# Performance work log

Measured on AMD Instinct MI355X. Metric: run time of the kernel, lower is better.

The kernel has to match this reference:

```python
import jax, jax.numpy as jnp
import numpy as np

B, T, E = 2, 2048, 1024
H, D = 8, 512
ROPE_BASE = 10000.0


def apply_rope(x):
    # x: [B, H, T, D] -- rotary positional embedding, half-split convention
    t = x.shape[2]
    d = x.shape[3]
    inv_freq = 1.0 / (ROPE_BASE ** (jnp.arange(0, d, 2, dtype=jnp.float32) / d))  # [D/2]
    ang = jnp.arange(t, dtype=jnp.float32)[:, None] * inv_freq[None, :]           # [T, D/2]
    cos = jnp.cos(ang)[None, None].astype(x.dtype)
    sin = jnp.sin(ang)[None, None].astype(x.dtype)
    x1, x2 = jnp.split(x, 2, axis=-1)
    return jnp.concatenate([x1 * cos - x2 * sin, x1 * sin + x2 * cos], axis=-1)


def setup_inputs() -> dict:
    key = jax.random.key(0)
    ks = jax.random.split(key, 5)
    s_in = 1.0 / np.sqrt(E)
    s_out = 1.0 / np.sqrt(H * D)
    return {
        "x": jax.random.normal(ks[0], (B, T, E), dtype=jnp.float32),
        "Wq": jax.random.normal(ks[1], (H * D, E), dtype=jnp.float32) * s_in,
        "Wk": jax.random.normal(ks[2], (H * D, E), dtype=jnp.float32) * s_in,
        "Wv": jax.random.normal(ks[3], (H * D, E), dtype=jnp.float32) * s_in,
        "Wo": jax.random.normal(ks[4], (E, H * D), dtype=jnp.float32) * s_out,
    }


def reference(x, Wq, Wk, Wv, Wo):
    b, t, e = x.shape
    # QKV projections (bias-free Linear: x @ W.T), reshape to [B, H, T, D]
    q = (x @ Wq.T).reshape(b, t, H, D).transpose(0, 2, 1, 3)
    k = (x @ Wk.T).reshape(b, t, H, D).transpose(0, 2, 1, 3)
    v = (x @ Wv.T).reshape(b, t, H, D).transpose(0, 2, 1, 3)
    # RoPE on q and k
    q = apply_rope(q)
    k = apply_rope(k)
    # scaled dot-product attention with causal mask
    scale = 1.0 / jnp.sqrt(jnp.asarray(D, dtype=x.dtype))
    scores = jnp.einsum("bhqd,bhkd->bhqk", q, k) * scale
    causal = jnp.tril(jnp.ones((t, t), dtype=bool))
    scores = jnp.where(causal[None, None], scores, jnp.asarray(-jnp.inf, dtype=scores.dtype))
    probs = jax.nn.softmax(scores, axis=-1)  # explicitly materialized, as in source
    attn = jnp.einsum("bhqk,bhkd->bhqd", probs, v)
    out = attn.transpose(0, 2, 1, 3).reshape(b, t, H * D) @ Wo.T
    return out
```

## Files before the change

kernel.cpp:

```cpp
#include <hip/hip_runtime.h>


#define DEV __device__ __forceinline__

using bf16x8  = __attribute__((ext_vector_type(8))) short;
using floatx4 = __attribute__((ext_vector_type(4))) float;

#define MFMA16(a, b, c) __builtin_amdgcn_mfma_f32_16x16x32_bf16((a), (b), (c), 0, 0, 0)

DEV unsigned short f2bf(float f) {
  union { float f; unsigned int u; } c; c.f = f;
  unsigned int u = c.u + 0x7FFFu + ((c.u >> 16) & 1u);
  return (unsigned short)(u >> 16);
}
DEV float bf2f(unsigned short h) {
  union { unsigned int u; float f; } c; c.u = ((unsigned int)h) << 16;
  return c.f;
}

DEV void ldsld16(const unsigned short* g, unsigned short* l) {
  __builtin_amdgcn_global_load_lds(
      (__attribute__((address_space(1))) void*)(g),
      (__attribute__((address_space(3))) void*)(l), 16, 0, 0);
}

__global__ void cast5_k(const float* __restrict__ x,  const float* __restrict__ wq,
                        const float* __restrict__ wk, const float* __restrict__ wv,
                        const float* __restrict__ wo,
                        unsigned short* __restrict__ xb,  unsigned short* __restrict__ wqb,
                        unsigned short* __restrict__ wkb, unsigned short* __restrict__ wvb,
                        unsigned short* __restrict__ wob) {
  const float* s; unsigned short* d;
  switch (blockIdx.y) {
    case 0: s = x;  d = xb;  break;
    case 1: s = wq; d = wqb; break;
    case 2: s = wk; d = wkb; break;
    case 3: s = wv; d = wvb; break;
    default: s = wo; d = wob; break;
  }
  int i = blockIdx.x * 256 + threadIdx.x;
  float4 v = ((const float4*)s)[i];
  uint2 o;
  o.x = (unsigned int)f2bf(v.x) | ((unsigned int)f2bf(v.y) << 16);
  o.y = (unsigned int)f2bf(v.z) | ((unsigned int)f2bf(v.w) << 16);
  ((uint2*)d)[i] = o;
}

__global__ __launch_bounds__(256) void qkv_gemm(
    const unsigned short* __restrict__ X,
    const unsigned short* __restrict__ Wq, const unsigned short* __restrict__ Wk,
    const unsigned short* __restrict__ Wv,
    unsigned short* __restrict__ Qo, unsigned short* __restrict__ Ko, unsigned short* __restrict__ Vo) {
  __shared__ __align__(16) unsigned short As[128 * 32];
  __shared__ __align__(16) unsigned short Bs[128 * 32];
  const int tid = threadIdx.x;
  const int wave = tid >> 6, lane = tid & 63, quad = lane >> 4, l16 = lane & 15;
  const int m0 = blockIdx.x * 128, n0 = blockIdx.y * 128;
  const int z = blockIdx.z;
  const unsigned short* W = (z == 0) ? Wq : (z == 1) ? Wk : Wv;
  const int wm = (wave >> 1) * 64, wn = (wave & 1) * 64;
  floatx4 acc[4][4];
#pragma unroll
  for (int i = 0; i < 4; ++i)
#pragma unroll
    for (int j = 0; j < 4; ++j) acc[i][j] = (floatx4){0.f, 0.f, 0.f, 0.f};

  const int r0 = wave * 32;
  const int lrow = lane >> 2, lchunk = (lane & 3) * 8;
  for (int k0 = 0; k0 < 1024; k0 += 32) {
    const unsigned short* ga = X + (size_t)(m0 + r0 + lrow) * 1024 + k0 + lchunk;
    const unsigned short* gb = W + (size_t)(n0 + r0 + lrow) * 1024 + k0 + lchunk;
    ldsld16(ga, As + r0 * 32);
    ldsld16(ga + (size_t)16 * 1024, As + r0 * 32 + 512);
    ldsld16(gb, Bs + r0 * 32);
    ldsld16(gb + (size_t)16 * 1024, Bs + r0 * 32 + 512);
    __syncthreads();
    bf16x8 af[4], bw[4];
#pragma unroll
    for (int i = 0; i < 4; ++i) af[i] = *(const bf16x8*)(As + (wm + i * 16 + l16) * 32 + quad * 8);
#pragma unroll
    for (int j = 0; j < 4; ++j) bw[j] = *(const bf16x8*)(Bs + (wn + j * 16 + l16) * 32 + quad * 8);
#pragma unroll
    for (int i = 0; i < 4; ++i)
#pragma unroll
      for (int j = 0; j < 4; ++j) acc[i][j] = MFMA16(af[i], bw[j], acc[i][j]);
    __syncthreads();
  }
#pragma unroll
  for (int i = 0; i < 4; ++i)
#pragma unroll
    for (int j = 0; j < 4; ++j) {
      int gn = n0 + wn + j * 16 + l16;
      int h = gn >> 9, d = gn & 511;
#pragma unroll
      for (int r = 0; r < 4; ++r) {
        int gm = m0 + wm + i * 16 + quad * 4 + r;
        int b = gm >> 11, t = gm & 2047;
        unsigned short v = f2bf(acc[i][j][r]);
        if (z == 2)
          Vo[((size_t)((b * 8 + h) * 512 + d)) * 2048 + t] = v;
        else
          ((z == 0) ? Qo : Ko)[((size_t)((b * 8 + h) * 2048 + t)) * 512 + d] = v;
      }
    }
}

__global__ void rope_k(unsigned short* __restrict__ Q, unsigned short* __restrict__ K) {
  int idx = blockIdx.x * 256 + threadIdx.x;
  unsigned short* P = (idx & 8388608) ? K : Q;
  int r = idx & 8388607;
  int row = r >> 8;
  int i = r & 255;
  int t = row & 2047;
  size_t base = (size_t)row * 512;
  float x1 = bf2f(P[base + i]);
  float x2 = bf2f(P[base + i + 256]);
  float freq = expf(-(float)i * 0.03597789207803197f);
  float ang = (float)t * freq;
  float sv, cv;
  sincosf(ang, &sv, &cv);
  P[base + i]       = f2bf(x1 * cv - x2 * sv);
  P[base + i + 256] = f2bf(x1 * sv + x2 * cv);
}

__global__ __launch_bounds__(256) void flash_attn(
    const unsigned short* __restrict__ Q, const unsigned short* __restrict__ K,
    const unsigned short* __restrict__ Vt, unsigned short* __restrict__ attn,
    unsigned short* __restrict__ P1, float* __restrict__ ml1, float* __restrict__ ml2,
    int split) {
  __shared__ __align__(16) unsigned short Ks[32 * 264];
  __shared__ __align__(16) unsigned short Vs[512 * 40];
  __shared__ __align__(16) unsigned short Ps[4 * 16 * 32];
  const int tid = threadIdx.x;
  const int wave = tid >> 6, lane = tid & 63, quad = lane >> 4, l16 = lane & 15;
  const int bh = blockIdx.x, b = bh >> 3, h = bh & 7;
  const int y = blockIdx.y;
  int qi, st0, stN, om;
  if (split) {
    if (y < 16)      { qi = 31 - y;  st0 = 0;  stN = 32;         om = 1; }
    else if (y < 32) { qi = 47 - y;  st0 = 32; stN = 2 * qi + 2; om = 2; }
    else             { qi = 47 - y;  st0 = 0;  stN = 2 * qi + 2; om = 0; }
  } else {
    qi = (y < 16) ? (31 - y) : (y - 16);
    st0 = 0; stN = 2 * qi + 2; om = 0;
  }
  const size_t bhoff = ((size_t)bh) << 20;
  const unsigned short* Qp = Q + bhoff;
  const unsigned short* Kp = K + bhoff;
  const unsigned short* Vp = Vt + bhoff;
  const int qb = qi * 64;

  bf16x8 qf[16];
  {
    const unsigned short* qrow = Qp + (size_t)(qb + wave * 16 + l16) * 512 + quad * 8;
#pragma unroll
    for (int ks = 0; ks < 16; ++ks) qf[ks] = *(const bf16x8*)(qrow + ks * 32);
  }
  floatx4 o[32];
#pragma unroll
  for (int n = 0; n < 32; ++n) o[n] = (floatx4){0.f, 0.f, 0.f, 0.f};
  float m_[4], l_[4];
#pragma unroll
  for (int r = 0; r < 4; ++r) { m_[r] = -3.0e38f; l_[r] = 0.f; }

  for (int st = st0; st < stN; ++st) {
    const int s0 = st * 32;
#pragma unroll
    for (int it = 0; it < 8; ++it) {
      int cid = it * 256 + tid;
      int d = cid >> 2, c = cid & 3;
      *(bf16x8*)(Vs + d * 40 + c * 8) = *(const bf16x8*)(Vp + (size_t)d * 2048 + s0 + c * 8);
    }
#pragma unroll
    for (int it = 0; it < 4; ++it) {
      int cid = it * 256 + tid;
      int row = cid >> 5, cc = cid & 31;
      *(bf16x8*)(Ks + row * 264 + cc * 8) = *(const bf16x8*)(Kp + (size_t)(s0 + row) * 512 + cc * 8);
    }
    __syncthreads();
    floatx4 sc0 = (floatx4){0.f, 0.f, 0.f, 0.f}, sc1 = sc0;
#pragma unroll
    for (int ks = 0; ks < 8; ++ks) {
      bf16x8 k0v = *(const bf16x8*)(Ks + l16 * 264 + ks * 32 + quad * 8);
      bf16x8 k1v = *(const bf16x8*)(Ks + (16 + l16) * 264 + ks * 32 + quad * 8);
      sc0 = MFMA16(qf[ks], k0v, sc0);
      sc1 = MFMA16(qf[ks], k1v, sc1);
    }
    __syncthreads();
#pragma unroll
    for (int it = 0; it < 4; ++it) {
      int cid = it * 256 + tid;
      int row = cid >> 5, cc = cid & 31;
      *(bf16x8*)(Ks + row * 264 + cc * 8) = *(const bf16x8*)(Kp + (size_t)(s0 + row) * 512 + 256 + cc * 8);
    }
    __syncthreads();
#pragma unroll
    for (int ks = 0; ks < 8; ++ks) {
      bf16x8 k0v = *(const bf16x8*)(Ks + l16 * 264 + ks * 32 + quad * 8);
      bf16x8 k1v = *(const bf16x8*)(Ks + (16 + l16) * 264 + ks * 32 + quad * 8);
      sc0 = MFMA16(qf[8 + ks], k0v, sc0);
      sc1 = MFMA16(qf[8 + ks], k1v, sc1);
    }
    const float scale = 0.04419417382415922f;
    const int qrow0 = qb + wave * 16 + quad * 4;
    float pr0[4], pr1[4], mr[4];
#pragma unroll
    for (int r = 0; r < 4; ++r) {
      float a0 = sc0[r] * scale, a1 = sc1[r] * scale;
      if (s0 + l16 > qrow0 + r) a0 = -3.0e38f;
      if (s0 + 16 + l16 > qrow0 + r) a1 = -3.0e38f;
      pr0[r] = a0; pr1[r] = a1;
      mr[r] = fmaxf(a0, a1);
    }
#pragma unroll
    for (int off = 1; off < 16; off <<= 1)
#pragma unroll
      for (int r = 0; r < 4; ++r) mr[r] = fmaxf(mr[r], __shfl_xor(mr[r], off, 64));
    float alpha[4], rs[4];
#pragma unroll
    for (int r = 0; r < 4; ++r) {
      float mn = fmaxf(m_[r], mr[r]);
      alpha[r] = __expf(m_[r] - mn);
      m_[r] = mn;
      float p0 = __expf(pr0[r] - mn);
      float p1 = __expf(pr1[r] - mn);
      rs[r] = p0 + p1;
      Ps[wave * 512 + (quad * 4 + r) * 32 + l16] = f2bf(p0);
      Ps[wave * 512 + (quad * 4 + r) * 32 + 16 + l16] = f2bf(p1);
    }
#pragma unroll
    for (int off = 1; off < 16; off <<= 1)
#pragma unroll
      for (int r = 0; r < 4; ++r) rs[r] += __shfl_xor(rs[r], off, 64);
#pragma unroll
    for (int r = 0; r < 4; ++r) l_[r] = l_[r] * alpha[r] + rs[r];
    if (__any(alpha[0] + alpha[1] + alpha[2] + alpha[3] < 4.0f)) {
#pragma unroll
      for (int n = 0; n < 32; ++n)
#pragma unroll
        for (int r = 0; r < 4; ++r) o[n][r] *= alpha[r];
    }
    bf16x8 pf = *(const bf16x8*)(Ps + wave * 512 + l16 * 32 + quad * 8);
#pragma unroll
    for (int nt = 0; nt < 32; ++nt) {
      bf16x8 vf = *(const bf16x8*)(Vs + (nt * 16 + l16) * 40 + quad * 8);
      o[nt] = MFMA16(pf, vf, o[nt]);
    }
    __syncthreads();
  }
  const int rowi = wave * 16 + quad * 4;
  if (om == 0) {
    float inv[4];
#pragma unroll
    for (int r = 0; r < 4; ++r) inv[r] = 1.0f / l_[r];
    unsigned short* arow = attn + ((size_t)(b * 2048 + qb + rowi)) * 4096 + h * 512 + l16;
#pragma unroll
    for (int nt = 0; nt < 32; ++nt)
#pragma unroll
      for (int r = 0; r < 4; ++r)
        arow[(size_t)r * 4096 + nt * 16] = f2bf(o[nt][r] * inv[r]);
  } else {
    const int p = bh * 16 + (qi - 16);
    float* ml = (om == 1) ? ml1 : ml2;
    if (l16 == 0) {
#pragma unroll
      for (int r = 0; r < 4; ++r) {
        ml[(size_t)p * 128 + (rowi + r) * 2]     = m_[r];
        ml[(size_t)p * 128 + (rowi + r) * 2 + 1] = l_[r];
      }
    }
    if (om == 1) {
      unsigned short* prow = P1 + ((size_t)p * 64 + rowi) * 512 + l16;
#pragma unroll
      for (int nt = 0; nt < 32; ++nt)
#pragma unroll
        for (int r = 0; r < 4; ++r)
          prow[(size_t)r * 512 + nt * 16] = f2bf(o[nt][r]);
    } else {
      unsigned short* arow = attn + ((size_t)(b * 2048 + qb + rowi)) * 4096 + h * 512 + l16;
#pragma unroll
      for (int nt = 0; nt < 32; ++nt)
#pragma unroll
        for (int r = 0; r < 4; ++r)
          arow[(size_t)r * 4096 + nt * 16] = f2bf(o[nt][r]);
    }
  }
}

__global__ void combine_k(const unsigned short* __restrict__ P1,
                          const float* __restrict__ ml1, const float* __restrict__ ml2,
                          unsigned short* __restrict__ attn) {
  const int p = blockIdx.x;
  const int bh = p >> 4, b = bh >> 3, h = bh & 7, qi = 16 + (p & 15);
  const int tid = threadIdx.x;
#pragma unroll
  for (int it = 0; it < 16; ++it) {
    int idx = it * 256 + tid;
    int r = idx >> 6, dc = idx & 63;
    float m1 = ml1[(size_t)p * 128 + r * 2], l1 = ml1[(size_t)p * 128 + r * 2 + 1];
    float m2 = ml2[(size_t)p * 128 + r * 2], l2 = ml2[(size_t)p * 128 + r * 2 + 1];
    float M = fmaxf(m1, m2);
    float w1 = __expf(m1 - M), w2 = __expf(m2 - M);
    float inv = 1.0f / (l1 * w1 + l2 * w2);
    const unsigned short* o1 = P1 + ((size_t)p * 64 + r) * 512 + dc * 8;
    unsigned short* ap = attn + ((size_t)(b * 2048 + qi * 64 + r)) * 4096 + h * 512 + dc * 8;
    unsigned short res[8];
#pragma unroll
    for (int j = 0; j < 8; ++j)
      res[j] = f2bf((bf2f(o1[j]) * w1 + bf2f(ap[j]) * w2) * inv);
    *(bf16x8*)ap = *(bf16x8*)res;
  }
}

__global__ __launch_bounds__(256) void out_gemm(
    const unsigned short* __restrict__ A, const unsigned short* __restrict__ W,
    float* __restrict__ C) {
  __shared__ __align__(16) unsigned short As[128 * 32];
  __shared__ __align__(16) unsigned short Bs[128 * 32];
  const int tid = threadIdx.x;
  const int wave = tid >> 6, lane = tid & 63, quad = lane >> 4, l16 = lane & 15;
  const int m0 = blockIdx.x * 128, n0 = blockIdx.y * 128;
  const int kb = blockIdx.z * 1024;
  const int wm = (wave >> 1) * 64, wn = (wave & 1) * 64;
  floatx4 acc[4][4];
#pragma unroll
  for (int i = 0; i < 4; ++i)
#pragma unroll
    for (int j = 0; j < 4; ++j) acc[i][j] = (floatx4){0.f, 0.f, 0.f, 0.f};
  const int r0 = wave * 32;
  const int lrow = lane >> 2, lchunk = (lane & 3) * 8;
  for (int k0 = kb; k0 < kb + 1024; k0 += 32) {
    const unsigned short* ga = A + (size_t)(m0 + r0 + lrow) * 4096 + k0 + lchunk;
    const unsigned short* gb = W + (size_t)(n0 + r0 + lrow) * 4096 + k0 + lchunk;
    ldsld16(ga, As + r0 * 32);
    ldsld16(ga + (size_t)16 * 4096, As + r0 * 32 + 512);
    ldsld16(gb, Bs + r0 * 32);
    ldsld16(gb + (size_t)16 * 4096, Bs + r0 * 32 + 512);
    __syncthreads();
    bf16x8 af[4], bw[4];
#pragma unroll
    for (int i = 0; i < 4; ++i) af[i] = *(const bf16x8*)(As + (wm + i * 16 + l16) * 32 + quad * 8);
#pragma unroll
    for (int j = 0; j < 4; ++j) bw[j] = *(const bf16x8*)(Bs + (wn + j * 16 + l16) * 32 + quad * 8);
#pragma unroll
    for (int i = 0; i < 4; ++i)
#pragma unroll
      for (int j = 0; j < 4; ++j) acc[i][j] = MFMA16(af[i], bw[j], acc[i][j]);
    __syncthreads();
  }
#pragma unroll
  for (int i = 0; i < 4; ++i)
#pragma unroll
    for (int j = 0; j < 4; ++j) {
      int gn = n0 + wn + j * 16 + l16;
#pragma unroll
      for (int r = 0; r < 4; ++r) {
        int gm = m0 + wm + i * 16 + quad * 4 + r;
        unsafeAtomicAdd(&C[(size_t)gm * 1024 + gn], acc[i][j][r]);
      }
    }
}

extern "C" void kernel_launch(void* const* d_in, const int* in_sizes, int n_in,
                              void* d_out, int out_size, void* d_ws, size_t ws_size,
                              hipStream_t stream) {
  const float* x  = (const float*)d_in[0];
  const float* Wq = (const float*)d_in[1];
  const float* Wk = (const float*)d_in[2];
  const float* Wv = (const float*)d_in[3];
  const float* Wo = (const float*)d_in[4];
  float* out = (float*)d_out;
  char* ws = (char*)d_ws;
  const size_t MB = 1048576;
  unsigned short* xb    = (unsigned short*)(ws + 0 * MB);
  unsigned short* wqb   = (unsigned short*)(ws + 8 * MB);
  unsigned short* wkb   = (unsigned short*)(ws + 16 * MB);
  unsigned short* wvb   = (unsigned short*)(ws + 24 * MB);
  unsigned short* wob   = (unsigned short*)(ws + 32 * MB);
  unsigned short* Qb    = (unsigned short*)(ws + 40 * MB);
  unsigned short* Kb    = (unsigned short*)(ws + 72 * MB);
  unsigned short* Vb    = (unsigned short*)(ws + 104 * MB);
  unsigned short* attnb = (unsigned short*)(ws + 0 * MB);
  unsigned short* P1    = (unsigned short*)(ws + 136 * MB);
  float* ml1            = (float*)(ws + 152 * MB);
  float* ml2            = (float*)(ws + 152 * MB + 131072);
  const int split = (ws_size >= (size_t)160 * MB) ? 1 : 0;

  hipMemsetAsync(d_out, 0, (size_t)4096 * 1024 * 4, stream);

  cast5_k<<<dim3(4096, 5), 256, 0, stream>>>(x, Wq, Wk, Wv, Wo, xb, wqb, wkb, wvb, wob);
  qkv_gemm<<<dim3(32, 32, 3), 256, 0, stream>>>(xb, wqb, wkb, wvb, Qb, Kb, Vb);
  rope_k<<<65536, 256, 0, stream>>>(Qb, Kb);
  flash_attn<<<dim3(16, split ? 48 : 32), 256, 0, stream>>>(Qb, Kb, Vb, attnb, P1, ml1, ml2, split);
  if (split) combine_k<<<256, 256, 0, stream>>>(P1, ml1, ml2, attnb);
  out_gemm<<<dim3(32, 8, 4), 256, 0, stream>>>(attnb, wob, out);
}
```

Before: 680.0 us.

## Restructure flash attention to 32-row tiles with split-D waves and slab V layout

The attention kernel now processes 32 query rows per block. Four waves split both the rows and the 512-wide head dimension, and each pair of waves sums its partial QK^T scores through shared memory. K fragments are read straight from global memory instead of being staged in LDS, and V is written by the QKV GEMM in 32-token slab blocks so each tile can be copied into LDS with asynchronous global_load_lds and prefetched for the next step. Split-K partitioning is rebalanced per q-tile, and occupancy is raised with launch_bounds(256,3). This trades extra block syncs, an LDS reduction and uncached direct K loads for lower register pressure, more blocks and less LDS staging.

```diff
diff --git a/kernel.cpp b/kernel.cpp
--- a/kernel.cpp
+++ b/kernel.cpp
@@ -92,15 +92,19 @@
     for (int j = 0; j < 4; ++j) {
       int gn = n0 + wn + j * 16 + l16;
       int h = gn >> 9, d = gn & 511;
-#pragma unroll
-      for (int r = 0; r < 4; ++r) {
-        int gm = m0 + wm + i * 16 + quad * 4 + r;
-        int b = gm >> 11, t = gm & 2047;
-        unsigned short v = f2bf(acc[i][j][r]);
-        if (z == 2)
-          Vo[((size_t)((b * 8 + h) * 512 + d)) * 2048 + t] = v;
-        else
-          ((z == 0) ? Qo : Ko)[((size_t)((b * 8 + h) * 2048 + t)) * 512 + d] = v;
+      int gm0 = m0 + wm + i * 16 + quad * 4;
+      int b = gm0 >> 11, t0 = gm0 & 2047;
+      if (z == 2) {
+        unsigned short pk[4];
+#pragma unroll
+        for (int r = 0; r < 4; ++r) pk[r] = f2bf(acc[i][j][r]);
+        size_t off = ((size_t)((b * 8 + h) * 64 + (t0 >> 5))) * 16384 + (size_t)d * 32 + (t0 & 31);
+        *(uint2*)(Vo + off) = *(uint2*)pk;
+      } else {
+        unsigned short* P = (z == 0) ? Qo : Ko;
+        size_t base = ((size_t)((b * 8 + h) * 2048 + t0)) * 512 + d;
+#pragma unroll
+        for (int r = 0; r < 4; ++r) P[base + (size_t)r * 512] = f2bf(acc[i][j][r]);
       }
     }
 }
@@ -123,93 +127,94 @@
   P[base + i + 256] = f2bf(x1 * sv + x2 * cv);
 }
 
-__global__ __launch_bounds__(256) void flash_attn(
+__global__ __launch_bounds__(256, 3) void flash_attn(
     const unsigned short* __restrict__ Q, const unsigned short* __restrict__ K,
-    const unsigned short* __restrict__ Vt, unsigned short* __restrict__ attn,
+    const unsigned short* __restrict__ Vslab, unsigned short* __restrict__ attn,
     unsigned short* __restrict__ P1, float* __restrict__ ml1, float* __restrict__ ml2,
     int split) {
-  __shared__ __align__(16) unsigned short Ks[32 * 264];
-  __shared__ __align__(16) unsigned short Vs[512 * 40];
-  __shared__ __align__(16) unsigned short Ps[4 * 16 * 32];
+  __shared__ __align__(16) unsigned short Vs[512 * 32];
+  __shared__ __align__(16) unsigned short Ps[2 * 512];
+  __shared__ __align__(16) float Sred[2 * 2 * 512];
   const int tid = threadIdx.x;
   const int wave = tid >> 6, lane = tid & 63, quad = lane >> 4, l16 = lane & 15;
-  const int bh = blockIdx.x, b = bh >> 3, h = bh & 7;
+  const int pr = wave >> 1, hh = wave & 1;
+  const int bh = blockIdx.x, b = bh >> 3, head = bh & 7;
   const int y = blockIdx.y;
   int qi, st0, stN, om;
   if (split) {
-    if (y < 16)      { qi = 31 - y;  st0 = 0;  stN = 32;         om = 1; }
-    else if (y < 32) { qi = 47 - y;  st0 = 32; stN = 2 * qi + 2; om = 2; }
-    else             { qi = 47 - y;  st0 = 0;  stN = 2 * qi + 2; om = 0; }
-  } else {
-    qi = (y < 16) ? (31 - y) : (y - 16);
-    st0 = 0; stN = 2 * qi + 2; om = 0;
-  }
-  const size_t bhoff = ((size_t)bh) << 20;
+    if (y < 64) {
+      qi = 63 - (y >> 1);
+      int mid = (qi + 1) >> 1;
+      if ((y & 1) == 0) { st0 = 0;   stN = mid;    om = 1; }
+      else              { st0 = mid; stN = qi + 1; om = 2; }
+    } else { qi = 95 - y; st0 = 0; stN = qi + 1; om = 0; }
+  } else { qi = 63 - y; st0 = 0; stN = qi + 1; om = 0; }
+
+  const size_t bhoff = (size_t)bh << 20;
   const unsigned short* Qp = Q + bhoff;
   const unsigned short* Kp = K + bhoff;
-  const unsigned short* Vp = Vt + bhoff;
-  const int qb = qi * 64;
-
-  bf16x8 qf[16];
+  const unsigned short* Vp = Vslab + bhoff;
+  const int qb = qi * 32;
+
+  bf16x8 qf[8];
   {
-    const unsigned short* qrow = Qp + (size_t)(qb + wave * 16 + l16) * 512 + quad * 8;
-#pragma unroll
-    for (int ks = 0; ks < 16; ++ks) qf[ks] = *(const bf16x8*)(qrow + ks * 32);
-  }
-  floatx4 o[32];
-#pragma unroll
-  for (int n = 0; n < 32; ++n) o[n] = (floatx4){0.f, 0.f, 0.f, 0.f};
+    const unsigned short* qrow = Qp + (size_t)(qb + pr * 16 + l16) * 512 + hh * 256 + quad * 8;
+#pragma unroll
+    for (int ks = 0; ks < 8; ++ks) qf[ks] = *(const bf16x8*)(qrow + ks * 32);
+  }
+  floatx4 o[16];
+#pragma unroll
+  for (int n = 0; n < 16; ++n) o[n] = (floatx4){0.f, 0.f, 0.f, 0.f};
   float m_[4], l_[4];
 #pragma unroll
   for (int r = 0; r < 4; ++r) { m_[r] = -3.0e38f; l_[r] = 0.f; }
+
+  {
+    const unsigned short* g = Vp + (size_t)st0 * 16384 + (size_t)(wave * 8) * 512 + lane * 8;
+    unsigned short* lp = Vs + wave * 8 * 512;
+#pragma unroll
+    for (int i = 0; i < 8; ++i) ldsld16(g + i * 512, lp + i * 512);
+  }
 
   for (int st = st0; st < stN; ++st) {
     const int s0 = st * 32;
-#pragma unroll
-    for (int it = 0; it < 8; ++it) {
-      int cid = it * 256 + tid;
-      int d = cid >> 2, c = cid & 3;
-      *(bf16x8*)(Vs + d * 40 + c * 8) = *(const bf16x8*)(Vp + (size_t)d * 2048 + s0 + c * 8);
-    }
-#pragma unroll
-    for (int it = 0; it < 4; ++it) {
-      int cid = it * 256 + tid;
-      int row = cid >> 5, cc = cid & 31;
-      *(bf16x8*)(Ks + row * 264 + cc * 8) = *(const bf16x8*)(Kp + (size_t)(s0 + row) * 512 + cc * 8);
-    }
-    __syncthreads();
     floatx4 sc0 = (floatx4){0.f, 0.f, 0.f, 0.f}, sc1 = sc0;
-#pragma unroll
-    for (int ks = 0; ks < 8; ++ks) {
-      bf16x8 k0v = *(const bf16x8*)(Ks + l16 * 264 + ks * 32 + quad * 8);
-      bf16x8 k1v = *(const bf16x8*)(Ks + (16 + l16) * 264 + ks * 32 + quad * 8);
-      sc0 = MFMA16(qf[ks], k0v, sc0);
-      sc1 = MFMA16(qf[ks], k1v, sc1);
-    }
-    __syncthreads();
-#pragma unroll
-    for (int it = 0; it < 4; ++it) {
-      int cid = it * 256 + tid;
-      int row = cid >> 5, cc = cid & 31;
-      *(bf16x8*)(Ks + row * 264 + cc * 8) = *(const bf16x8*)(Kp + (size_t)(s0 + row) * 512 + 256 + cc * 8);
-    }
-    __syncthreads();
-#pragma unroll
-    for (int ks = 0; ks < 8; ++ks) {
-      bf16x8 k0v = *(const bf16x8*)(Ks + l16 * 264 + ks * 32 + quad * 8);
-      bf16x8 k1v = *(const bf16x8*)(Ks + (16 + l16) * 264 + ks * 32 + quad * 8);
-      sc0 = MFMA16(qf[8 + ks], k0v, sc0);
-      sc1 = MFMA16(qf[8 + ks], k1v, sc1);
+    const unsigned short* kbase = Kp + hh * 256 + quad * 8;
+#pragma unroll
+    for (int half = 0; half < 2; ++half) {
+      bf16x8 kb[8];
+#pragma unroll
+      for (int q4 = 0; q4 < 4; ++q4) {
+        int ks = half * 4 + q4;
+        kb[q4 * 2]     = *(const bf16x8*)(kbase + (size_t)(s0 + l16) * 512 + ks * 32);
+        kb[q4 * 2 + 1] = *(const bf16x8*)(kbase + (size_t)(s0 + 16 + l16) * 512 + ks * 32);
+      }
+#pragma unroll
+      for (int q4 = 0; q4 < 4; ++q4) {
+        sc0 = MFMA16(qf[half * 4 + q4], kb[q4 * 2], sc0);
+        sc1 = MFMA16(qf[half * 4 + q4], kb[q4 * 2 + 1], sc1);
+      }
+    }
+    float* sw = Sred + (pr * 2 + hh) * 512;
+    *(floatx4*)(sw + l16 * 16 + quad * 4) = sc0;
+    *(floatx4*)(sw + (16 + l16) * 16 + quad * 4) = sc1;
+    __syncthreads();
+    {
+      const float* srd = Sred + (pr * 2 + (1 - hh)) * 512;
+      floatx4 r0 = *(const floatx4*)(srd + l16 * 16 + quad * 4);
+      floatx4 r1 = *(const floatx4*)(srd + (16 + l16) * 16 + quad * 4);
+#pragma unroll
+      for (int r = 0; r < 4; ++r) { sc0[r] += r0[r]; sc1[r] += r1[r]; }
     }
     const float scale = 0.04419417382415922f;
-    const int qrow0 = qb + wave * 16 + quad * 4;
-    float pr0[4], pr1[4], mr[4];
+    const int qrow0 = qb + pr * 16 + quad * 4;
+    float pv0[4], pv1[4], mr[4];
 #pragma unroll
     for (int r = 0; r < 4; ++r) {
       float a0 = sc0[r] * scale, a1 = sc1[r] * scale;
       if (s0 + l16 > qrow0 + r) a0 = -3.0e38f;
       if (s0 + 16 + l16 > qrow0 + r) a1 = -3.0e38f;
-      pr0[r] = a0; pr1[r] = a1;
+      pv0[r] = a0; pv1[r] = a1;
       mr[r] = fmaxf(a0, a1);
     }
 #pragma unroll
@@ -222,11 +227,10 @@
       float mn = fmaxf(m_[r], mr[r]);
       alpha[r] = __expf(m_[r] - mn);
       m_[r] = mn;
-      float p0 = __expf(pr0[r] - mn);
-      float p1 = __expf(pr1[r] - mn);
+      float p0 = __expf(pv0[r] - mn);
+      float p1 = __expf(pv1[r] - mn);
       rs[r] = p0 + p1;
-      Ps[wave * 512 + (quad * 4 + r) * 32 + l16] = f2bf(p0);
-      Ps[wave * 512 + (quad * 4 + r) * 32 + 16 + l16] = f2bf(p1);
+      Ps[pr * 512 + (quad * 4 + r) * 32 + hh * 16 + l16] = f2bf(hh ? p1 : p0);
     }
 #pragma unroll
     for (int off = 1; off < 16; off <<= 1)
@@ -234,55 +238,62 @@
       for (int r = 0; r < 4; ++r) rs[r] += __shfl_xor(rs[r], off, 64);
 #pragma unroll
     for (int r = 0; r < 4; ++r) l_[r] = l_[r] * alpha[r] + rs[r];
+    __syncthreads();
     if (__any(alpha[0] + alpha[1] + alpha[2] + alpha[3] < 4.0f)) {
 #pragma unroll
-      for (int n = 0; n < 32; ++n)
+      for (int n = 0; n < 16; ++n)
 #pragma unroll
         for (int r = 0; r < 4; ++r) o[n][r] *= alpha[r];
     }
-    bf16x8 pf = *(const bf16x8*)(Ps + wave * 512 + l16 * 32 + quad * 8);
-#pragma unroll
-    for (int nt = 0; nt < 32; ++nt) {
-      bf16x8 vf = *(const bf16x8*)(Vs + (nt * 16 + l16) * 40 + quad * 8);
+    bf16x8 pf = *(const bf16x8*)(Ps + pr * 512 + l16 * 32 + quad * 8);
+#pragma unroll
+    for (int nt = 0; nt < 16; ++nt) {
+      bf16x8 vf = *(const bf16x8*)(Vs + (size_t)(hh * 256 + nt * 16 + l16) * 32 + quad * 8);
       o[nt] = MFMA16(pf, vf, o[nt]);
     }
     __syncthreads();
-  }
-  const int rowi = wave * 16 + quad * 4;
-  if (om == 0) {
-    float inv[4];
-#pragma unroll
-    for (int r = 0; r < 4; ++r) inv[r] = 1.0f / l_[r];
-    unsigned short* arow = attn + ((size_t)(b * 2048 + qb + rowi)) * 4096 + h * 512 + l16;
-#pragma unroll
-    for (int nt = 0; nt < 32; ++nt)
+    if (st + 1 < stN) {
+      const unsigned short* g = Vp + (size_t)(st + 1) * 16384 + (size_t)(wave * 8) * 512 + lane * 8;
+      unsigned short* lp = Vs + wave * 8 * 512;
+#pragma unroll
+      for (int i = 0; i < 8; ++i) ldsld16(g + i * 512, lp + i * 512);
+    }
+  }
+  const int rbase = pr * 16 + quad * 4;
+  int p1i = bh * 32 + (qi - 32);
+  if (om == 1) {
+    unsigned short* prow = P1 + ((size_t)p1i * 32 + rbase) * 512 + hh * 256 + l16;
+#pragma unroll
+    for (int nt = 0; nt < 16; ++nt)
 #pragma unroll
       for (int r = 0; r < 4; ++r)
-        arow[(size_t)r * 4096 + nt * 16] = f2bf(o[nt][r] * inv[r]);
+        prow[(size_t)r * 512 + nt * 16] = f2bf(o[nt][r]);
   } else {
-    const int p = bh * 16 + (qi - 16);
-    float* ml = (om == 1) ? ml1 : ml2;
-    if (l16 == 0) {
-#pragma unroll
-      for (int r = 0; r < 4; ++r) {
-        ml[(size_t)p * 128 + (rowi + r) * 2]     = m_[r];
-        ml[(size_t)p * 128 + (rowi + r) * 2 + 1] = l_[r];
-      }
-    }
-    if (om == 1) {
-      unsigned short* prow = P1 + ((size_t)p * 64 + rowi) * 512 + l16;
-#pragma unroll
-      for (int nt = 0; nt < 32; ++nt)
+    unsigned short* arow =
+        attn + ((size_t)(b * 2048 + qb + rbase)) * 4096 + head * 512 + hh * 256 + l16;
+    if (om == 0) {
+      float inv[4];
+#pragma unroll
+      for (int r = 0; r < 4; ++r) inv[r] = 1.0f / l_[r];
+#pragma unroll
+      for (int nt = 0; nt < 16; ++nt)
 #pragma unroll
         for (int r = 0; r < 4; ++r)
-          prow[(size_t)r * 512 + nt * 16] = f2bf(o[nt][r]);
+          arow[(size_t)r * 4096 + nt * 16] = f2bf(o[nt][r] * inv[r]);
     } else {
-      unsigned short* arow = attn + ((size_t)(b * 2048 + qb + rowi)) * 4096 + h * 512 + l16;
-#pragma unroll
-      for (int nt = 0; nt < 32; ++nt)
+#pragma unroll
+      for (int nt = 0; nt < 16; ++nt)
 #pragma unroll
         for (int r = 0; r < 4; ++r)
           arow[(size_t)r * 4096 + nt * 16] = f2bf(o[nt][r]);
+    }
+  }
+  if (om != 0 && hh == 0 && l16 == 0) {
+    float* ml = (om == 1) ? ml1 : ml2;
+#pragma unroll
+    for (int r = 0; r < 4; ++r) {
+      ml[(size_t)p1i * 64 + (rbase + r) * 2]     = m_[r];
+      ml[(size_t)p1i * 64 + (rbase + r) * 2 + 1] = l_[r];
     }
   }
 }
@@ -291,19 +302,19 @@
                           const float* __restrict__ ml1, const float* __restrict__ ml2,
                           unsigned short* __restrict__ attn) {
   const int p = blockIdx.x;
-  const int bh = p >> 4, b = bh >> 3, h = bh & 7, qi = 16 + (p & 15);
+  const int bh = p >> 5, qi = 32 + (p & 31), b = bh >> 3, head = bh & 7;
   const int tid = threadIdx.x;
 #pragma unroll
-  for (int it = 0; it < 16; ++it) {
+  for (int it = 0; it < 8; ++it) {
     int idx = it * 256 + tid;
-    int r = idx >> 6, dc = idx & 63;
-    float m1 = ml1[(size_t)p * 128 + r * 2], l1 = ml1[(size_t)p * 128 + r * 2 + 1];
-    float m2 = ml2[(size_t)p * 128 + r * 2], l2 = ml2[(size_t)p * 128 + r * 2 + 1];
+    int row = idx >> 6, c8 = (idx & 63) * 8;
+    float m1 = ml1[(size_t)p * 64 + row * 2], l1 = ml1[(size_t)p * 64 + row * 2 + 1];
+    float m2 = ml2[(size_t)p * 64 + row * 2], l2 = ml2[(size_t)p * 64 + row * 2 + 1];
     float M = fmaxf(m1, m2);
     float w1 = __expf(m1 - M), w2 = __expf(m2 - M);
     float inv = 1.0f / (l1 * w1 + l2 * w2);
-    const unsigned short* o1 = P1 + ((size_t)p * 64 + r) * 512 + dc * 8;
-    unsigned short* ap = attn + ((size_t)(b * 2048 + qi * 64 + r)) * 4096 + h * 512 + dc * 8;
+    const unsigned short* o1 = P1 + ((size_t)p * 32 + row) * 512 + c8;
+    unsigned short* ap = attn + ((size_t)(b * 2048 + qi * 32 + row)) * 4096 + head * 512 + c8;
     unsigned short res[8];
 #pragma unroll
     for (int j = 0; j < 8; ++j)
@@ -391,7 +402,7 @@
   cast5_k<<<dim3(4096, 5), 256, 0, stream>>>(x, Wq, Wk, Wv, Wo, xb, wqb, wkb, wvb, wob);
   qkv_gemm<<<dim3(32, 32, 3), 256, 0, stream>>>(xb, wqb, wkb, wvb, Qb, Kb, Vb);
   rope_k<<<65536, 256, 0, stream>>>(Qb, Kb);
-  flash_attn<<<dim3(16, split ? 48 : 32), 256, 0, stream>>>(Qb, Kb, Vb, attnb, P1, ml1, ml2, split);
-  if (split) combine_k<<<256, 256, 0, stream>>>(P1, ml1, ml2, attnb);
+  flash_attn<<<dim3(16, split ? 96 : 64), 256, 0, stream>>>(Qb, Kb, Vb, attnb, P1, ml1, ml2, split);
+  if (split) combine_k<<<512, 256, 0, stream>>>(P1, ml1, ml2, attnb);
   out_gemm<<<dim3(32, 8, 4), 256, 0, stream>>>(attnb, wob, out);
 }
```

After: 704.4 us. +3.6%, slower.

## Pre-tile K/V into padded LDS layout and async-prefetch tiles in flash attention

Applied to the files above, without the earlier changes.

The QKV GEMM now writes K and V straight into a per-tile padded layout that matches the attention kernel's LDS layout. The attention kernel can then fill LDS with direct global-to-LDS loads of the whole 32x512 K tile at once, and it prefetches the next tile after each iteration's compute. This removes the split K halves, the extra barriers and the register-staged copies. It also pads the P buffer, sets launch_bounds for two blocks, and moves the Wo cast later so workspace can be reused. The cost is more LDS per block, and the next-tile loads overlap only with the loop tail, since the barrier sits at the loop top.

```diff
diff --git a/kernel.cpp b/kernel.cpp
--- a/kernel.cpp
+++ b/kernel.cpp
@@ -7,6 +7,12 @@
 using floatx4 = __attribute__((ext_vector_type(4))) float;
 
 #define MFMA16(a, b, c) __builtin_amdgcn_mfma_f32_16x16x32_bf16((a), (b), (c), 0, 0, 0)
+
+#define KT_BH 1097728
+#define KT_TILE 17152
+#define KT_ROW 536
+#define VT_BH 1310720
+#define VT_TILE 20480
 
 DEV unsigned short f2bf(float f) {
   union { float f; unsigned int u; } c; c.f = f;
@@ -24,20 +30,26 @@
       (__attribute__((address_space(3))) void*)(l), 16, 0, 0);
 }
 
-__global__ void cast5_k(const float* __restrict__ x,  const float* __restrict__ wq,
+__global__ void cast4_k(const float* __restrict__ x,  const float* __restrict__ wq,
                         const float* __restrict__ wk, const float* __restrict__ wv,
-                        const float* __restrict__ wo,
                         unsigned short* __restrict__ xb,  unsigned short* __restrict__ wqb,
-                        unsigned short* __restrict__ wkb, unsigned short* __restrict__ wvb,
-                        unsigned short* __restrict__ wob) {
+                        unsigned short* __restrict__ wkb, unsigned short* __restrict__ wvb) {
   const float* s; unsigned short* d;
   switch (blockIdx.y) {
     case 0: s = x;  d = xb;  break;
     case 1: s = wq; d = wqb; break;
     case 2: s = wk; d = wkb; break;
-    case 3: s = wv; d = wvb; break;
-    default: s = wo; d = wob; break;
-  }
+    default: s = wv; d = wvb; break;
+  }
+  int i = blockIdx.x * 256 + threadIdx.x;
+  float4 v = ((const float4*)s)[i];
+  uint2 o;
+  o.x = (unsigned int)f2bf(v.x) | ((unsigned int)f2bf(v.y) << 16);
+  o.y = (unsigned int)f2bf(v.z) | ((unsigned int)f2bf(v.w) << 16);
+  ((uint2*)d)[i] = o;
+}
+
+__global__ void cast1_k(const float* __restrict__ s, unsigned short* __restrict__ d) {
   int i = blockIdx.x * 256 + threadIdx.x;
   float4 v = ((const float4*)s)[i];
   uint2 o;
@@ -92,27 +104,43 @@
     for (int j = 0; j < 4; ++j) {
       int gn = n0 + wn + j * 16 + l16;
       int h = gn >> 9, d = gn & 511;
-#pragma unroll
-      for (int r = 0; r < 4; ++r) {
-        int gm = m0 + wm + i * 16 + quad * 4 + r;
-        int b = gm >> 11, t = gm & 2047;
-        unsigned short v = f2bf(acc[i][j][r]);
-        if (z == 2)
-          Vo[((size_t)((b * 8 + h) * 512 + d)) * 2048 + t] = v;
-        else
-          ((z == 0) ? Qo : Ko)[((size_t)((b * 8 + h) * 2048 + t)) * 512 + d] = v;
+      int gm0 = m0 + wm + i * 16 + quad * 4;
+      int b = gm0 >> 11, t0 = gm0 & 2047;
+      int bh = b * 8 + h;
+      if (z == 2) {
+        unsigned short pk[4];
+#pragma unroll
+        for (int r = 0; r < 4; ++r) pk[r] = f2bf(acc[i][j][r]);
+        size_t off = (size_t)bh * VT_BH + (t0 >> 5) * VT_TILE + (size_t)d * 40 + (t0 & 31);
+        *(uint2*)(Vo + off) = *(uint2*)pk;
+      } else if (z == 1) {
+        size_t off = (size_t)bh * KT_BH + (t0 >> 5) * KT_TILE + (size_t)(t0 & 31) * KT_ROW + d;
+#pragma unroll
+        for (int r = 0; r < 4; ++r) Ko[off + (size_t)r * KT_ROW] = f2bf(acc[i][j][r]);
+      } else {
+        size_t base = ((size_t)(bh * 2048 + t0)) * 512 + d;
+#pragma unroll
+        for (int r = 0; r < 4; ++r) Qo[base + (size_t)r * 512] = f2bf(acc[i][j][r]);
       }
     }
 }
 
-__global__ void rope_k(unsigned short* __restrict__ Q, unsigned short* __restrict__ K) {
+__global__ void rope_k(unsigned short* __restrict__ Q, unsigned short* __restrict__ Kt) {
   int idx = blockIdx.x * 256 + threadIdx.x;
-  unsigned short* P = (idx & 8388608) ? K : Q;
   int r = idx & 8388607;
   int row = r >> 8;
   int i = r & 255;
   int t = row & 2047;
-  size_t base = (size_t)row * 512;
+  unsigned short* P;
+  size_t base;
+  if (idx & 8388608) {
+    int bh = row >> 11;
+    base = (size_t)bh * KT_BH + (t >> 5) * KT_TILE + (size_t)(t & 31) * KT_ROW;
+    P = Kt;
+  } else {
+    base = (size_t)row * 512;
+    P = Q;
+  }
   float x1 = bf2f(P[base + i]);
   float x2 = bf2f(P[base + i + 256]);
   float freq = expf(-(float)i * 0.03597789207803197f);
@@ -123,31 +151,28 @@
   P[base + i + 256] = f2bf(x1 * sv + x2 * cv);
 }
 
-__global__ __launch_bounds__(256) void flash_attn(
-    const unsigned short* __restrict__ Q, const unsigned short* __restrict__ K,
+__global__ __launch_bounds__(256, 2) void flash_attn(
+    const unsigned short* __restrict__ Q, const unsigned short* __restrict__ Kt,
     const unsigned short* __restrict__ Vt, unsigned short* __restrict__ attn,
     unsigned short* __restrict__ P1, float* __restrict__ ml1, float* __restrict__ ml2,
     int split) {
-  __shared__ __align__(16) unsigned short Ks[32 * 264];
+  __shared__ __align__(16) unsigned short Ks[32 * 536];
   __shared__ __align__(16) unsigned short Vs[512 * 40];
-  __shared__ __align__(16) unsigned short Ps[4 * 16 * 32];
+  __shared__ __align__(16) unsigned short Ps[4 * 16 * 40];
   const int tid = threadIdx.x;
   const int wave = tid >> 6, lane = tid & 63, quad = lane >> 4, l16 = lane & 15;
-  const int bh = blockIdx.x, b = bh >> 3, h = bh & 7;
+  const int bh = blockIdx.x, b = bh >> 3, head = bh & 7;
   const int y = blockIdx.y;
   int qi, st0, stN, om;
   if (split) {
-    if (y < 16)      { qi = 31 - y;  st0 = 0;  stN = 32;         om = 1; }
-    else if (y < 32) { qi = 47 - y;  st0 = 32; stN = 2 * qi + 2; om = 2; }
-    else             { qi = 47 - y;  st0 = 0;  stN = 2 * qi + 2; om = 0; }
-  } else {
-    qi = (y < 16) ? (31 - y) : (y - 16);
-    st0 = 0; stN = 2 * qi + 2; om = 0;
-  }
-  const size_t bhoff = ((size_t)bh) << 20;
-  const unsigned short* Qp = Q + bhoff;
-  const unsigned short* Kp = K + bhoff;
-  const unsigned short* Vp = Vt + bhoff;
+    if (y < 16)      { qi = 31 - y; st0 = 0;  stN = 32;         om = 1; }
+    else if (y < 32) { qi = 47 - y; st0 = 32; stN = 2 * qi + 2; om = 2; }
+    else             { qi = 47 - y; st0 = 0;  stN = 2 * qi + 2; om = 0; }
+  } else { qi = (y < 16) ? (31 - y) : (y - 16); st0 = 0; stN = 2 * qi + 2; om = 0; }
+
+  const unsigned short* Qp = Q + ((size_t)bh << 20);
+  const unsigned short* Kp = Kt + (size_t)bh * KT_BH;
+  const unsigned short* Vp = Vt + (size_t)bh * VT_BH;
   const int qb = qi * 64;
 
   bf16x8 qf[16];
@@ -163,53 +188,43 @@
 #pragma unroll
   for (int r = 0; r < 4; ++r) { m_[r] = -3.0e38f; l_[r] = 0.f; }
 
+  unsigned short* psw = Ps + wave * 640;
+
+  {
+    const unsigned short* gk = Kp + (size_t)st0 * KT_TILE;
+    const unsigned short* gv = Vp + (size_t)st0 * VT_TILE;
+#pragma unroll
+    for (int j = 0; j < 9; ++j) {
+      int c0 = wave * 536 + j * 64;
+      if (j < 8 || lane < 24) ldsld16(gk + (size_t)(c0 + lane) * 8, Ks + c0 * 8);
+    }
+#pragma unroll
+    for (int j = 0; j < 10; ++j) {
+      int c0 = wave * 640 + j * 64;
+      ldsld16(gv + (size_t)(c0 + lane) * 8, Vs + c0 * 8);
+    }
+  }
+
   for (int st = st0; st < stN; ++st) {
+    __syncthreads();
     const int s0 = st * 32;
-#pragma unroll
-    for (int it = 0; it < 8; ++it) {
-      int cid = it * 256 + tid;
-      int d = cid >> 2, c = cid & 3;
-      *(bf16x8*)(Vs + d * 40 + c * 8) = *(const bf16x8*)(Vp + (size_t)d * 2048 + s0 + c * 8);
-    }
-#pragma unroll
-    for (int it = 0; it < 4; ++it) {
-      int cid = it * 256 + tid;
-      int row = cid >> 5, cc = cid & 31;
-      *(bf16x8*)(Ks + row * 264 + cc * 8) = *(const bf16x8*)(Kp + (size_t)(s0 + row) * 512 + cc * 8);
-    }
-    __syncthreads();
     floatx4 sc0 = (floatx4){0.f, 0.f, 0.f, 0.f}, sc1 = sc0;
 #pragma unroll
-    for (int ks = 0; ks < 8; ++ks) {
-      bf16x8 k0v = *(const bf16x8*)(Ks + l16 * 264 + ks * 32 + quad * 8);
-      bf16x8 k1v = *(const bf16x8*)(Ks + (16 + l16) * 264 + ks * 32 + quad * 8);
-      sc0 = MFMA16(qf[ks], k0v, sc0);
-      sc1 = MFMA16(qf[ks], k1v, sc1);
-    }
-    __syncthreads();
-#pragma unroll
-    for (int it = 0; it < 4; ++it) {
-      int cid = it * 256 + tid;
-      int row = cid >> 5, cc = cid & 31;
-      *(bf16x8*)(Ks + row * 264 + cc * 8) = *(const bf16x8*)(Kp + (size_t)(s0 + row) * 512 + 256 + cc * 8);
-    }
-    __syncthreads();
-#pragma unroll
-    for (int ks = 0; ks < 8; ++ks) {
-      bf16x8 k0v = *(const bf16x8*)(Ks + l16 * 264 + ks * 32 + quad * 8);
-      bf16x8 k1v = *(const bf16x8*)(Ks + (16 + l16) * 264 + ks * 32 + quad * 8);
-      sc0 = MFMA16(qf[8 + ks], k0v, sc0);
-      sc1 = MFMA16(qf[8 + ks], k1v, sc1);
+    for (int ks = 0; ks < 16; ++ks) {
+      bf16x8 k0 = *(const bf16x8*)(Ks + (size_t)l16 * 536 + ks * 32 + quad * 8);
+      bf16x8 k1 = *(const bf16x8*)(Ks + (size_t)(16 + l16) * 536 + ks * 32 + quad * 8);
+      sc0 = MFMA16(qf[ks], k0, sc0);
+      sc1 = MFMA16(qf[ks], k1, sc1);
     }
     const float scale = 0.04419417382415922f;
     const int qrow0 = qb + wave * 16 + quad * 4;
-    float pr0[4], pr1[4], mr[4];
+    float pv0[4], pv1[4], mr[4];
 #pragma unroll
     for (int r = 0; r < 4; ++r) {
       float a0 = sc0[r] * scale, a1 = sc1[r] * scale;
       if (s0 + l16 > qrow0 + r) a0 = -3.0e38f;
       if (s0 + 16 + l16 > qrow0 + r) a1 = -3.0e38f;
-      pr0[r] = a0; pr1[r] = a1;
+      pv0[r] = a0; pv1[r] = a1;
       mr[r] = fmaxf(a0, a1);
     }
 #pragma unroll
@@ -222,11 +237,11 @@
       float mn = fmaxf(m_[r], mr[r]);
       alpha[r] = __expf(m_[r] - mn);
       m_[r] = mn;
-      float p0 = __expf(pr0[r] - mn);
-      float p1 = __expf(pr1[r] - mn);
+      float p0 = __expf(pv0[r] - mn);
+      float p1 = __expf(pv1[r] - mn);
       rs[r] = p0 + p1;
-      Ps[wave * 512 + (quad * 4 + r) * 32 + l16] = f2bf(p0);
-      Ps[wave * 512 + (quad * 4 + r) * 32 + 16 + l16] = f2bf(p1);
+      psw[(quad * 4 + r) * 40 + l16] = f2bf(p0);
+      psw[(quad * 4 + r) * 40 + 16 + l16] = f2bf(p1);
     }
 #pragma unroll
     for (int off = 1; off < 16; off <<= 1)
@@ -240,20 +255,34 @@
 #pragma unroll
         for (int r = 0; r < 4; ++r) o[n][r] *= alpha[r];
     }
-    bf16x8 pf = *(const bf16x8*)(Ps + wave * 512 + l16 * 32 + quad * 8);
+    bf16x8 pf = *(const bf16x8*)(psw + (size_t)l16 * 40 + quad * 8);
 #pragma unroll
     for (int nt = 0; nt < 32; ++nt) {
-      bf16x8 vf = *(const bf16x8*)(Vs + (nt * 16 + l16) * 40 + quad * 8);
+      bf16x8 vf = *(const bf16x8*)(Vs + (size_t)(nt * 16 + l16) * 40 + quad * 8);
       o[nt] = MFMA16(pf, vf, o[nt]);
     }
     __syncthreads();
+    if (st + 1 < stN) {
+      const unsigned short* gk = Kp + (size_t)(st + 1) * KT_TILE;
+      const unsigned short* gv = Vp + (size_t)(st + 1) * VT_TILE;
+#pragma unroll
+      for (int j = 0; j < 9; ++j) {
+        int c0 = wave * 536 + j * 64;
+        if (j < 8 || lane < 24) ldsld16(gk + (size_t)(c0 + lane) * 8, Ks + c0 * 8);
+      }
+#pragma unroll
+      for (int j = 0; j < 10; ++j) {
+        int c0 = wave * 640 + j * 64;
+        ldsld16(gv + (size_t)(c0 + lane) * 8, Vs + c0 * 8);
+      }
+    }
   }
   const int rowi = wave * 16 + quad * 4;
   if (om == 0) {
     float inv[4];
 #pragma unroll
     for (int r = 0; r < 4; ++r) inv[r] = 1.0f / l_[r];
-    unsigned short* arow = attn + ((size_t)(b * 2048 + qb + rowi)) * 4096 + h * 512 + l16;
+    unsigned short* arow = attn + ((size_t)(b * 2048 + qb + rowi)) * 4096 + head * 512 + l16;
 #pragma unroll
     for (int nt = 0; nt < 32; ++nt)
 #pragma unroll
@@ -277,7 +306,7 @@
         for (int r = 0; r < 4; ++r)
           prow[(size_t)r * 512 + nt * 16] = f2bf(o[nt][r]);
     } else {
-      unsigned short* arow = attn + ((size_t)(b * 2048 + qb + rowi)) * 4096 + h * 512 + l16;
+      unsigned short* arow = attn + ((size_t)(b * 2048 + qb + rowi)) * 4096 + head * 512 + l16;
 #pragma unroll
       for (int nt = 0; nt < 32; ++nt)
 #pragma unroll
@@ -291,19 +320,19 @@
                           const float* __restrict__ ml1, const float* __restrict__ ml2,
                           unsigned short* __restrict__ attn) {
   const int p = blockIdx.x;
-  const int bh = p >> 4, b = bh >> 3, h = bh & 7, qi = 16 + (p & 15);
+  const int bh = p >> 4, b = bh >> 3, head = bh & 7, qi = 16 + (p & 15);
   const int tid = threadIdx.x;
 #pragma unroll
   for (int it = 0; it < 16; ++it) {
     int idx = it * 256 + tid;
-    int r = idx >> 6, dc = idx & 63;
-    float m1 = ml1[(size_t)p * 128 + r * 2], l1 = ml1[(size_t)p * 128 + r * 2 + 1];
-    float m2 = ml2[(size_t)p * 128 + r * 2], l2 = ml2[(size_t)p * 128 + r * 2 + 1];
+    int row = idx >> 6, c8 = (idx & 63) * 8;
+    float m1 = ml1[(size_t)p * 128 + row * 2], l1 = ml1[(size_t)p * 128 + row * 2 + 1];
+    float m2 = ml2[(size_t)p * 128 + row * 2], l2 = ml2[(size_t)p * 128 + row * 2 + 1];
     float M = fmaxf(m1, m2);
     float w1 = __expf(m1 - M), w2 = __expf(m2 - M);
     float inv = 1.0f / (l1 * w1 + l2 * w2);
-    const unsigned short* o1 = P1 + ((size_t)p * 64 + r) * 512 + dc * 8;
-    unsigned short* ap = attn + ((size_t)(b * 2048 + qi * 64 + r)) * 4096 + h * 512 + dc * 8;
+    const unsigned short* o1 = P1 + ((size_t)p * 64 + row) * 512 + c8;
+    unsigned short* ap = attn + ((size_t)(b * 2048 + qi * 64 + row)) * 4096 + head * 512 + c8;
     unsigned short res[8];
 #pragma unroll
     for (int j = 0; j < 8; ++j)
@@ -376,22 +405,23 @@
   unsigned short* wqb   = (unsigned short*)(ws + 8 * MB);
   unsigned short* wkb   = (unsigned short*)(ws + 16 * MB);
   unsigned short* wvb   = (unsigned short*)(ws + 24 * MB);
+  unsigned short* attnb = (unsigned short*)(ws + 0 * MB);
+  unsigned short* Qb    = (unsigned short*)(ws + 32 * MB);
   unsigned short* wob   = (unsigned short*)(ws + 32 * MB);
-  unsigned short* Qb    = (unsigned short*)(ws + 40 * MB);
-  unsigned short* Kb    = (unsigned short*)(ws + 72 * MB);
-  unsigned short* Vb    = (unsigned short*)(ws + 104 * MB);
-  unsigned short* attnb = (unsigned short*)(ws + 0 * MB);
-  unsigned short* P1    = (unsigned short*)(ws + 136 * MB);
-  float* ml1            = (float*)(ws + 152 * MB);
-  float* ml2            = (float*)(ws + 152 * MB + 131072);
+  unsigned short* Ktb   = (unsigned short*)(ws + 64 * MB);
+  unsigned short* Vtb   = (unsigned short*)(ws + 98 * MB);
+  unsigned short* P1    = (unsigned short*)(ws + 138 * MB);
+  float* ml1            = (float*)(ws + 154 * MB);
+  float* ml2            = (float*)(ws + 154 * MB + 131072);
   const int split = (ws_size >= (size_t)160 * MB) ? 1 : 0;
 
   hipMemsetAsync(d_out, 0, (size_t)4096 * 1024 * 4, stream);
 
-  cast5_k<<<dim3(4096, 5), 256, 0, stream>>>(x, Wq, Wk, Wv, Wo, xb, wqb, wkb, wvb, wob);
-  qkv_gemm<<<dim3(32, 32, 3), 256, 0, stream>>>(xb, wqb, wkb, wvb, Qb, Kb, Vb);
-  rope_k<<<65536, 256, 0, stream>>>(Qb, Kb);
-  flash_attn<<<dim3(16, split ? 48 : 32), 256, 0, stream>>>(Qb, Kb, Vb, attnb, P1, ml1, ml2, split);
+  cast4_k<<<dim3(4096, 4), 256, 0, stream>>>(x, Wq, Wk, Wv, xb, wqb, wkb, wvb);
+  qkv_gemm<<<dim3(32, 32, 3), 256, 0, stream>>>(xb, wqb, wkb, wvb, Qb, Ktb, Vtb);
+  rope_k<<<65536, 256, 0, stream>>>(Qb, Ktb);
+  flash_attn<<<dim3(16, split ? 48 : 32), 256, 0, stream>>>(Qb, Ktb, Vtb, attnb, P1, ml1, ml2, split);
   if (split) combine_k<<<256, 256, 0, stream>>>(P1, ml1, ml2, attnb);
+  cast1_k<<<4096, 256, 0, stream>>>(Wo, wob);
   out_gemm<<<dim3(32, 8, 4), 256, 0, stream>>>(attnb, wob, out);
 }
```

Measured after the change: 702.2 us. +3.3%, slower.
